# Kernel optimization log

Hardware: AMD Instinct MI355X
Metric: run time of the kernel (lower is better)

Reference implementation:

```python
import jax, jax.numpy as jnp
import numpy as np

B, N, C = 1, 131072, 128
BS, H = 32, 4          # block_size, num_heads
HD = C // H            # head_dim = 32
NB = N // BS           # num_blocks = 4096
NEG = -1e30            # stand-in for -inf (identical softmax result, safe grads)


def setup_inputs() -> dict:
    key = jax.random.key(0)
    ks = jax.random.split(key, 8)
    x = jax.random.normal(ks[0], (B, N, C), jnp.float32)
    edge_feats = jax.random.normal(ks[1], (NB, BS, BS + 1, 4), jnp.float32)
    # 0/1 connectivity mask; guarantee self (diagonal) and global-token column are attendable
    attn_mask = jax.random.randint(ks[2], (NB, BS, BS + 1), 0, 2).astype(jnp.int32)
    attn_mask = attn_mask.at[:, :, BS].set(1)
    d = jnp.arange(BS)
    attn_mask = attn_mask.at[:, d, d].set(1)
    # parameters (torch nn.Linear layout: weight [out, in])
    Wqkv = jax.random.normal(ks[3], (3 * C, C), jnp.float32) * (C ** -0.5)
    bqkv = jnp.zeros((3 * C,), jnp.float32)
    Wproj = jax.random.normal(ks[4], (C, C), jnp.float32) * (C ** -0.5)
    bproj = jnp.zeros((C,), jnp.float32)
    Wgate = jax.random.normal(ks[5], (H, 4), jnp.float32) * 0.01  # init std=0.01
    bgate = jnp.zeros((H,), jnp.float32)
    return dict(x=x, edge_feats=edge_feats, Wqkv=Wqkv, bqkv=bqkv,
                Wproj=Wproj, bproj=bproj, Wgate=Wgate, bgate=bgate,
                attn_mask=attn_mask)


def reference(x, edge_feats, Wqkv, bqkv, Wproj, bproj, Wgate, bgate, attn_mask):
    scale = HD ** -0.5
    x_blk = x.reshape(B, NB, BS, C)
    # global token per block = block mean
    block_node = x_blk.mean(axis=2, keepdims=True)          # [B,NB,1,C]
    kv = jnp.concatenate([x_blk, block_node], axis=2)       # [B,NB,BS+1,C]
    # qkv projections (slice the fused weight like the torch code slices outputs)
    q = (x_blk @ Wqkv[:C].T + bqkv[:C]).reshape(B, NB, BS, H, HD)
    k = (kv @ Wqkv[C:2 * C].T + bqkv[C:2 * C]).reshape(B, NB, BS + 1, H, HD)
    v = (kv @ Wqkv[2 * C:].T + bqkv[2 * C:]).reshape(B, NB, BS + 1, H, HD)
    scores = jnp.einsum('bnqhd,bnkhd->bnqkh', q, k) * scale  # [B,NB,BS,BS+1,H]
    # physics bias: overwrite global-token column and diagonal with (0,0,0,1)
    self_row = jnp.array([0.0, 0.0, 0.0, 1.0], jnp.float32)
    bp = jnp.broadcast_to(edge_feats[None], (B, NB, BS, BS + 1, 4))
    bp = bp.at[:, :, :, BS, :].set(self_row)
    d = jnp.arange(BS)
    bp = bp.at[:, :, d, d, :].set(self_row)
    scores = scores + bp[..., 3:4]                           # additive physics bias
    m = attn_mask[None, :, :, :, None] != 0                  # [1,NB,BS,BS+1,1]
    scores = jnp.where(m, scores, NEG)
    attn_probs = jax.nn.softmax(scores, axis=3)
    # additive edge gate (masked to 0 where disconnected)
    lew = jnp.where(m, bp @ Wgate.T + bgate, 0.0)            # [B,NB,BS,BS+1,H]
    combined = attn_probs + lew
    x_out = jnp.einsum('bnqkh,bnkhd->bnqhd', combined, v).reshape(B, N, C)
    return x_out @ Wproj.T + bproj
```

## Files before the change

kernel.cpp:

```cpp
#include <hip/hip_runtime.h>
#include <hip/hip_bf16.h>

#define NBLK 4096
#define BS 32
#define CH 128

typedef float f32x4 __attribute__((ext_vector_type(4)));
typedef short bf16x8 __attribute__((ext_vector_type(8)));
typedef unsigned short u16x4 __attribute__((ext_vector_type(4)));

__device__ __forceinline__ short f2b(float x) {
    union { float f; unsigned u; } c; c.f = x;
    unsigned r = c.u + 0x7fffu + ((c.u >> 16) & 1u);
    return (short)(r >> 16);
}
__device__ __forceinline__ float b2f(unsigned short h) {
    union { unsigned u; float f; } c; c.u = ((unsigned)h) << 16; return c.f;
}
__device__ __forceinline__ u16x4 pack4(f32x4 a) {
    u16x4 o;
    o[0] = (unsigned short)f2b(a[0]);
    o[1] = (unsigned short)f2b(a[1]);
    o[2] = (unsigned short)f2b(a[2]);
    o[3] = (unsigned short)f2b(a[3]);
    return o;
}

__global__ void convert_weights(const float* __restrict__ wqkv,
                                const float* __restrict__ wproj,
                                short* __restrict__ wsout) {
    int i = blockIdx.x * 256 + threadIdx.x;
    if (i < 3 * CH * CH) {
        wsout[i] = f2b(wqkv[i]);
    } else {
        int j = i - 3 * CH * CH;
        if (j < CH * CH) wsout[3 * CH * CH + j] = f2b(wproj[j]);
    }
}

__launch_bounds__(256, 4)
__global__ void fused_block_attn(
    const float* __restrict__ x,
    const float* __restrict__ edge_feats,
    const float* __restrict__ bqkv,
    const float* __restrict__ bproj,
    const float* __restrict__ wgate,
    const float* __restrict__ bgate,
    const int*   __restrict__ attn_mask,
    const short* __restrict__ wqkv_b,
    const short* __restrict__ wproj_b,
    float* __restrict__ out)
{
    const int b    = blockIdx.x;
    const int tid  = threadIdx.x;
    const int lane = tid & 63;
    const int w    = tid >> 6;
    const int lm   = lane & 15;
    const int g    = lane >> 4;
    const int ak   = g * 8;
    const int rb   = g * 4;

    __shared__ short regionA[32 * 136];
    __shared__ short qs[4 * 32 * 40];
    __shared__ short kc[4 * 32 * 40];
    __shared__ short vt[4 * 32 * 40];

    const float* xb = x + (size_t)b * BS * CH;
    #pragma unroll
    for (int it = 0; it < 4; ++it) {
        int idx = tid + it * 256;
        int r   = idx >> 5;
        int c4  = idx & 31;
        f32x4 t = ((const f32x4*)xb)[idx];
        *(u16x4*)&regionA[r * 136 + c4 * 4] = pack4(t);
    }
    __syncthreads();

    bf16x8 kvf[2][4];
    #pragma unroll
    for (int kk = 0; kk < 4; ++kk) {
        kvf[0][kk] = *(const bf16x8*)&regionA[lm * 136 + kk * 32 + ak];
        kvf[1][kk] = *(const bf16x8*)&regionA[(16 + lm) * 136 + kk * 32 + ak];
    }

    #pragma unroll
    for (int ntl = 0; ntl < 6; ++ntl) {
        const int nt = w * 6 + ntl;
        const int o0 = nt * 16;
        const short* wp = wqkv_b + (o0 + lm) * CH + ak;
        bf16x8 wf[4];
        #pragma unroll
        for (int kk = 0; kk < 4; ++kk) wf[kk] = *(const bf16x8*)(wp + kk * 32);

        const int h  = (o0 >> 5) & 3;
        if (nt < 16) {
            f32x4 a0 = *(const f32x4*)(bqkv + o0 + rb);
            f32x4 a1 = a0;
            #pragma unroll
            for (int kk = 0; kk < 4; ++kk) {
                a0 = __builtin_amdgcn_mfma_f32_16x16x32_bf16(wf[kk], kvf[0][kk], a0, 0, 0, 0);
                a1 = __builtin_amdgcn_mfma_f32_16x16x32_bf16(wf[kk], kvf[1][kk], a1, 0, 0, 0);
            }
            const int d0 = (o0 & 31) + rb;
            short* dst = ((nt < 8) ? qs : kc) + h * 1280;
            *(u16x4*)&dst[lm * 40 + d0]        = pack4(a0);
            *(u16x4*)&dst[(16 + lm) * 40 + d0] = pack4(a1);
        } else {
            float bv = bqkv[o0 + lm];
            f32x4 a0 = {bv, bv, bv, bv};
            f32x4 a1 = a0;
            #pragma unroll
            for (int kk = 0; kk < 4; ++kk) {
                a0 = __builtin_amdgcn_mfma_f32_16x16x32_bf16(kvf[0][kk], wf[kk], a0, 0, 0, 0);
                a1 = __builtin_amdgcn_mfma_f32_16x16x32_bf16(kvf[1][kk], wf[kk], a1, 0, 0, 0);
            }
            const int d0 = (o0 & 31) + lm;
            short* dst = vt + h * 1280;
            *(u16x4*)&dst[d0 * 40 + rb]      = pack4(a0);
            *(u16x4*)&dst[d0 * 40 + 16 + rb] = pack4(a1);
        }
    }
    __syncthreads();

    {
        const int h = w;
        const short* ksh = kc + h * 1280;
        const short* qsh = qs + h * 1280;
        bf16x8 af0 = *(const bf16x8*)&ksh[lm * 40 + ak];
        bf16x8 af1 = *(const bf16x8*)&ksh[(16 + lm) * 40 + ak];
        bf16x8 bf0 = *(const bf16x8*)&qsh[lm * 40 + ak];
        bf16x8 bf1 = *(const bf16x8*)&qsh[(16 + lm) * 40 + ak];
        f32x4 z = {0.f, 0.f, 0.f, 0.f};
        f32x4 s00 = __builtin_amdgcn_mfma_f32_16x16x32_bf16(af0, bf0, z, 0, 0, 0);
        f32x4 s10 = __builtin_amdgcn_mfma_f32_16x16x32_bf16(af1, bf0, z, 0, 0, 0);
        f32x4 s01 = __builtin_amdgcn_mfma_f32_16x16x32_bf16(af0, bf1, z, 0, 0, 0);
        f32x4 s11 = __builtin_amdgcn_mfma_f32_16x16x32_bf16(af1, bf1, z, 0, 0, 0);
        const float SC = 0.17677669529663689f;
        short* ch = kc + h * 1280;
        *(u16x4*)&ch[lm * 40 + rb]             = pack4(s00 * SC);
        *(u16x4*)&ch[lm * 40 + 16 + rb]        = pack4(s10 * SC);
        *(u16x4*)&ch[(16 + lm) * 40 + rb]      = pack4(s01 * SC);
        *(u16x4*)&ch[(16 + lm) * 40 + 16 + rb] = pack4(s11 * SC);
    }
    __syncthreads();

    {
        const int r    = tid >> 3;
        const int h    = (tid >> 1) & 3;
        const int half = tid & 1;
        short* ch = kc + h * 1280;

        bf16x8 t0 = *(const bf16x8*)&ch[r * 40 + half * 16];
        bf16x8 t1 = *(const bf16x8*)&ch[r * 40 + half * 16 + 8];
        float d[16];
        #pragma unroll
        for (int j = 0; j < 8; ++j) { d[j] = b2f((unsigned short)t0[j]); d[8 + j] = b2f((unsigned short)t1[j]); }

        float sd = 0.f;
        #pragma unroll
        for (int j = 0; j < 16; ++j) sd += d[j];
        sd += __shfl_xor(sd, 1);
        const float d32 = sd * 0.03125f;

        const float* efb = edge_feats + ((size_t)(b * BS + r)) * 33 * 4 + half * 64;
        const int*   mk  = attn_mask + (size_t)(b * BS + r) * 33 + half * 16;
        f32x4 wg = *(const f32x4*)(wgate + h * 4);
        float bg = bgate[h];

        float sc[16], lw[16];
        float mx = -3.0e38f;
        #pragma unroll
        for (int s = 0; s < 16; ++s) {
            int sg = half * 16 + s;
            f32x4 ef = *(const f32x4*)(efb + s * 4);
            if (sg == r) { ef[0] = 0.f; ef[1] = 0.f; ef[2] = 0.f; ef[3] = 1.f; }
            int m = mk[s];
            sc[s] = m ? (d[s] + ef[3]) : -1.0e30f;
            lw[s] = m ? (ef[0] * wg[0] + ef[1] * wg[1] + ef[2] * wg[2] + ef[3] * wg[3] + bg) : 0.f;
            mx = fmaxf(mx, sc[s]);
        }
        mx = fmaxf(mx, __shfl_xor(mx, 1));
        const float sc32 = d32 + 1.0f;
        mx = fmaxf(mx, sc32);

        float se = 0.f;
        #pragma unroll
        for (int s = 0; s < 16; ++s) {
            float e = __expf(sc[s] - mx);
            sc[s] = e;
            se += e;
        }
        const float e32 = __expf(sc32 - mx);
        const float tot = se + __shfl_xor(se, 1) + e32;
        const float rinv = 1.0f / tot;
        const float add32 = (e32 * rinv + (wg[3] + bg)) * 0.03125f;

        #pragma unroll
        for (int pk = 0; pk < 4; ++pk) {
            u16x4 o;
            #pragma unroll
            for (int j = 0; j < 4; ++j) {
                float v = sc[pk * 4 + j] * rinv + lw[pk * 4 + j] + add32;
                o[j] = (unsigned short)f2b(v);
            }
            *(u16x4*)&ch[r * 40 + half * 16 + pk * 4] = o;
        }
    }
    __syncthreads();

    {
        const int h = w;
        const short* ch  = kc + h * 1280;
        const short* vth = vt + h * 1280;
        bf16x8 av0 = *(const bf16x8*)&vth[lm * 40 + ak];
        bf16x8 av1 = *(const bf16x8*)&vth[(16 + lm) * 40 + ak];
        bf16x8 bc0 = *(const bf16x8*)&ch[lm * 40 + ak];
        bf16x8 bc1 = *(const bf16x8*)&ch[(16 + lm) * 40 + ak];
        f32x4 z = {0.f, 0.f, 0.f, 0.f};
        f32x4 x00 = __builtin_amdgcn_mfma_f32_16x16x32_bf16(av0, bc0, z, 0, 0, 0);
        f32x4 x10 = __builtin_amdgcn_mfma_f32_16x16x32_bf16(av1, bc0, z, 0, 0, 0);
        f32x4 x01 = __builtin_amdgcn_mfma_f32_16x16x32_bf16(av0, bc1, z, 0, 0, 0);
        f32x4 x11 = __builtin_amdgcn_mfma_f32_16x16x32_bf16(av1, bc1, z, 0, 0, 0);
        short* xob = regionA;
        *(u16x4*)&xob[lm * 136 + h * 32 + rb]             = pack4(x00);
        *(u16x4*)&xob[lm * 136 + h * 32 + 16 + rb]        = pack4(x10);
        *(u16x4*)&xob[(16 + lm) * 136 + h * 32 + rb]      = pack4(x01);
        *(u16x4*)&xob[(16 + lm) * 136 + h * 32 + 16 + rb] = pack4(x11);
    }
    __syncthreads();

    {
        const short* xob = regionA;
        bf16x8 a2[2][4];
        #pragma unroll
        for (int kk = 0; kk < 4; ++kk) {
            a2[0][kk] = *(const bf16x8*)&xob[lm * 136 + kk * 32 + ak];
            a2[1][kk] = *(const bf16x8*)&xob[(16 + lm) * 136 + kk * 32 + ak];
        }
        float* ob = out + (size_t)b * BS * CH;
        #pragma unroll
        for (int ntl = 0; ntl < 2; ++ntl) {
            int col = (w * 2 + ntl) * 16 + lm;
            float bias = bproj[col];
            f32x4 acc0 = {bias, bias, bias, bias};
            f32x4 acc1 = acc0;
            #pragma unroll
            for (int kk = 0; kk < 4; ++kk) {
                bf16x8 bfr = *(const bf16x8*)(wproj_b + col * CH + kk * 32 + ak);
                acc0 = __builtin_amdgcn_mfma_f32_16x16x32_bf16(a2[0][kk], bfr, acc0, 0, 0, 0);
                acc1 = __builtin_amdgcn_mfma_f32_16x16x32_bf16(a2[1][kk], bfr, acc1, 0, 0, 0);
            }
            #pragma unroll
            for (int j = 0; j < 4; ++j) {
                ob[(rb + j) * CH + col]      = acc0[j];
                ob[(16 + rb + j) * CH + col] = acc1[j];
            }
        }
    }
}

extern "C" void kernel_launch(void* const* d_in, const int* in_sizes, int n_in,
                              void* d_out, int out_size, void* d_ws, size_t ws_size,
                              hipStream_t stream) {
    const float* x          = (const float*)d_in[0];
    const float* edge_feats = (const float*)d_in[1];
    const float* Wqkv       = (const float*)d_in[2];
    const float* bqkv       = (const float*)d_in[3];
    const float* Wproj      = (const float*)d_in[4];
    const float* bproj      = (const float*)d_in[5];
    const float* Wgate      = (const float*)d_in[6];
    const float* bgate      = (const float*)d_in[7];
    const int*   attn_mask  = (const int*)d_in[8];
    float* out = (float*)d_out;
    short* wb  = (short*)d_ws;

    convert_weights<<<256, 256, 0, stream>>>(Wqkv, Wproj, wb);
    fused_block_attn<<<NBLK, 256, 0, stream>>>(
        x, edge_feats, bqkv, bproj, Wgate, bgate, attn_mask,
        wb, wb + 3 * CH * CH, out);
}
```

Baseline: 95.87 us.

## Give each wave one head end-to-end to drop most block barriers

Each wave now computes Q, K and V for its own head straight from global x, which is converted to bf16 in registers. Scores, softmax and PV then run wave-locally in XOR-swizzled shared-memory tiles, leaving only one __syncthreads before the output projection. The change also drops the softmax max-subtraction, prefetches the projection weights before the barrier, uses the builtin bf16 conversion, and raises launch bounds to 6 blocks per SM. The cost is redundant global reads of x by each wave, and exp overflow becomes possible if scores grow large.

```diff
diff --git a/kernel.cpp b/kernel.cpp
--- a/kernel.cpp
+++ b/kernel.cpp
@@ -10,20 +10,25 @@
 typedef unsigned short u16x4 __attribute__((ext_vector_type(4)));
 
 __device__ __forceinline__ short f2b(float x) {
-    union { float f; unsigned u; } c; c.f = x;
-    unsigned r = c.u + 0x7fffu + ((c.u >> 16) & 1u);
-    return (short)(r >> 16);
+    return __builtin_bit_cast(short, __float2bfloat16(x));
 }
 __device__ __forceinline__ float b2f(unsigned short h) {
     union { unsigned u; float f; } c; c.u = ((unsigned)h) << 16; return c.f;
 }
 __device__ __forceinline__ u16x4 pack4(f32x4 a) {
     u16x4 o;
-    o[0] = (unsigned short)f2b(a[0]);
-    o[1] = (unsigned short)f2b(a[1]);
-    o[2] = (unsigned short)f2b(a[2]);
-    o[3] = (unsigned short)f2b(a[3]);
+    o[0] = (unsigned short)f2b(a[0]); o[1] = (unsigned short)f2b(a[1]);
+    o[2] = (unsigned short)f2b(a[2]); o[3] = (unsigned short)f2b(a[3]);
     return o;
+}
+__device__ __forceinline__ bf16x8 pack8(f32x4 a, f32x4 b) {
+    bf16x8 o;
+    o[0] = f2b(a[0]); o[1] = f2b(a[1]); o[2] = f2b(a[2]); o[3] = f2b(a[3]);
+    o[4] = f2b(b[0]); o[5] = f2b(b[1]); o[6] = f2b(b[2]); o[7] = f2b(b[3]);
+    return o;
+}
+__device__ __forceinline__ int swz(int row, int col) {
+    return (row << 5) + ((((col >> 3) ^ ((row >> 1) & 3)) << 3) | (col & 7));
 }
 
 __global__ void convert_weights(const float* __restrict__ wqkv,
@@ -38,7 +43,7 @@
     }
 }
 
-__launch_bounds__(256, 4)
+__launch_bounds__(256, 6)
 __global__ void fused_block_attn(
     const float* __restrict__ x,
     const float* __restrict__ edge_feats,
@@ -60,195 +65,173 @@
     const int ak   = g * 8;
     const int rb   = g * 4;
 
-    __shared__ short regionA[32 * 136];
-    __shared__ short qs[4 * 32 * 40];
-    __shared__ short kc[4 * 32 * 40];
-    __shared__ short vt[4 * 32 * 40];
-
-    const float* xb = x + (size_t)b * BS * CH;
-    #pragma unroll
-    for (int it = 0; it < 4; ++it) {
-        int idx = tid + it * 256;
-        int r   = idx >> 5;
-        int c4  = idx & 31;
-        f32x4 t = ((const f32x4*)xb)[idx];
-        *(u16x4*)&regionA[r * 136 + c4 * 4] = pack4(t);
-    }
-    __syncthreads();
-
+    __shared__ short Rv[4096];
+    __shared__ short Rq[4096];
+    __shared__ short Rk[4096];
+    short* vt = Rv + w * 1024;
+    short* qc = Rq + w * 1024;
+    short* kc = Rk + w * 1024;
+
+    const float* xb = x + (size_t)b * (BS * CH);
     bf16x8 kvf[2][4];
     #pragma unroll
     for (int kk = 0; kk < 4; ++kk) {
-        kvf[0][kk] = *(const bf16x8*)&regionA[lm * 136 + kk * 32 + ak];
-        kvf[1][kk] = *(const bf16x8*)&regionA[(16 + lm) * 136 + kk * 32 + ak];
-    }
-
-    #pragma unroll
-    for (int ntl = 0; ntl < 6; ++ntl) {
-        const int nt = w * 6 + ntl;
-        const int o0 = nt * 16;
+        const float* p0 = xb + lm * CH + kk * 32 + ak;
+        const float* p1 = p0 + 16 * CH;
+        kvf[0][kk] = pack8(*(const f32x4*)p0, *(const f32x4*)(p0 + 4));
+        kvf[1][kk] = pack8(*(const f32x4*)p1, *(const f32x4*)(p1 + 4));
+    }
+
+    #pragma unroll
+    for (int t = 0; t < 4; ++t) {
+        const int o0 = ((t >> 1) ? CH : 0) + w * 32 + (t & 1) * 16;
         const short* wp = wqkv_b + (o0 + lm) * CH + ak;
         bf16x8 wf[4];
         #pragma unroll
         for (int kk = 0; kk < 4; ++kk) wf[kk] = *(const bf16x8*)(wp + kk * 32);
-
-        const int h  = (o0 >> 5) & 3;
-        if (nt < 16) {
-            f32x4 a0 = *(const f32x4*)(bqkv + o0 + rb);
-            f32x4 a1 = a0;
-            #pragma unroll
-            for (int kk = 0; kk < 4; ++kk) {
-                a0 = __builtin_amdgcn_mfma_f32_16x16x32_bf16(wf[kk], kvf[0][kk], a0, 0, 0, 0);
-                a1 = __builtin_amdgcn_mfma_f32_16x16x32_bf16(wf[kk], kvf[1][kk], a1, 0, 0, 0);
-            }
-            const int d0 = (o0 & 31) + rb;
-            short* dst = ((nt < 8) ? qs : kc) + h * 1280;
-            *(u16x4*)&dst[lm * 40 + d0]        = pack4(a0);
-            *(u16x4*)&dst[(16 + lm) * 40 + d0] = pack4(a1);
-        } else {
-            float bv = bqkv[o0 + lm];
-            f32x4 a0 = {bv, bv, bv, bv};
-            f32x4 a1 = a0;
-            #pragma unroll
-            for (int kk = 0; kk < 4; ++kk) {
-                a0 = __builtin_amdgcn_mfma_f32_16x16x32_bf16(kvf[0][kk], wf[kk], a0, 0, 0, 0);
-                a1 = __builtin_amdgcn_mfma_f32_16x16x32_bf16(kvf[1][kk], wf[kk], a1, 0, 0, 0);
-            }
-            const int d0 = (o0 & 31) + lm;
-            short* dst = vt + h * 1280;
-            *(u16x4*)&dst[d0 * 40 + rb]      = pack4(a0);
-            *(u16x4*)&dst[d0 * 40 + 16 + rb] = pack4(a1);
-        }
-    }
-    __syncthreads();
-
-    {
-        const int h = w;
-        const short* ksh = kc + h * 1280;
-        const short* qsh = qs + h * 1280;
-        bf16x8 af0 = *(const bf16x8*)&ksh[lm * 40 + ak];
-        bf16x8 af1 = *(const bf16x8*)&ksh[(16 + lm) * 40 + ak];
-        bf16x8 bf0 = *(const bf16x8*)&qsh[lm * 40 + ak];
-        bf16x8 bf1 = *(const bf16x8*)&qsh[(16 + lm) * 40 + ak];
+        f32x4 acc0 = *(const f32x4*)(bqkv + o0 + rb);
+        f32x4 acc1 = acc0;
+        #pragma unroll
+        for (int kk = 0; kk < 4; ++kk) {
+            acc0 = __builtin_amdgcn_mfma_f32_16x16x32_bf16(wf[kk], kvf[0][kk], acc0, 0, 0, 0);
+            acc1 = __builtin_amdgcn_mfma_f32_16x16x32_bf16(wf[kk], kvf[1][kk], acc1, 0, 0, 0);
+        }
+        short* dst = (t >> 1) ? kc : qc;
+        const int c0 = (t & 1) * 16 + rb;
+        *(u16x4*)&dst[swz(lm, c0)]      = pack4(acc0);
+        *(u16x4*)&dst[swz(16 + lm, c0)] = pack4(acc1);
+    }
+    #pragma unroll
+    for (int t = 0; t < 2; ++t) {
+        const int o0 = 2 * CH + w * 32 + t * 16;
+        const short* wp = wqkv_b + (o0 + lm) * CH + ak;
+        bf16x8 wf[4];
+        #pragma unroll
+        for (int kk = 0; kk < 4; ++kk) wf[kk] = *(const bf16x8*)(wp + kk * 32);
+        float bv = bqkv[o0 + lm];
+        f32x4 acc0 = {bv, bv, bv, bv};
+        f32x4 acc1 = acc0;
+        #pragma unroll
+        for (int kk = 0; kk < 4; ++kk) {
+            acc0 = __builtin_amdgcn_mfma_f32_16x16x32_bf16(kvf[0][kk], wf[kk], acc0, 0, 0, 0);
+            acc1 = __builtin_amdgcn_mfma_f32_16x16x32_bf16(kvf[1][kk], wf[kk], acc1, 0, 0, 0);
+        }
+        const int row = t * 16 + lm;
+        *(u16x4*)&vt[swz(row, rb)]      = pack4(acc0);
+        *(u16x4*)&vt[swz(row, 16 + rb)] = pack4(acc1);
+    }
+
+    {
+        bf16x8 af0 = *(const bf16x8*)&kc[swz(lm, ak)];
+        bf16x8 af1 = *(const bf16x8*)&kc[swz(16 + lm, ak)];
+        bf16x8 bq0 = *(const bf16x8*)&qc[swz(lm, ak)];
+        bf16x8 bq1 = *(const bf16x8*)&qc[swz(16 + lm, ak)];
         f32x4 z = {0.f, 0.f, 0.f, 0.f};
-        f32x4 s00 = __builtin_amdgcn_mfma_f32_16x16x32_bf16(af0, bf0, z, 0, 0, 0);
-        f32x4 s10 = __builtin_amdgcn_mfma_f32_16x16x32_bf16(af1, bf0, z, 0, 0, 0);
-        f32x4 s01 = __builtin_amdgcn_mfma_f32_16x16x32_bf16(af0, bf1, z, 0, 0, 0);
-        f32x4 s11 = __builtin_amdgcn_mfma_f32_16x16x32_bf16(af1, bf1, z, 0, 0, 0);
+        f32x4 s00 = __builtin_amdgcn_mfma_f32_16x16x32_bf16(af0, bq0, z, 0, 0, 0);
+        f32x4 s10 = __builtin_amdgcn_mfma_f32_16x16x32_bf16(af1, bq0, z, 0, 0, 0);
+        f32x4 s01 = __builtin_amdgcn_mfma_f32_16x16x32_bf16(af0, bq1, z, 0, 0, 0);
+        f32x4 s11 = __builtin_amdgcn_mfma_f32_16x16x32_bf16(af1, bq1, z, 0, 0, 0);
         const float SC = 0.17677669529663689f;
-        short* ch = kc + h * 1280;
-        *(u16x4*)&ch[lm * 40 + rb]             = pack4(s00 * SC);
-        *(u16x4*)&ch[lm * 40 + 16 + rb]        = pack4(s10 * SC);
-        *(u16x4*)&ch[(16 + lm) * 40 + rb]      = pack4(s01 * SC);
-        *(u16x4*)&ch[(16 + lm) * 40 + 16 + rb] = pack4(s11 * SC);
-    }
-    __syncthreads();
-
-    {
-        const int r    = tid >> 3;
-        const int h    = (tid >> 1) & 3;
-        const int half = tid & 1;
-        short* ch = kc + h * 1280;
-
-        bf16x8 t0 = *(const bf16x8*)&ch[r * 40 + half * 16];
-        bf16x8 t1 = *(const bf16x8*)&ch[r * 40 + half * 16 + 8];
-        float d[16];
-        #pragma unroll
-        for (int j = 0; j < 8; ++j) { d[j] = b2f((unsigned short)t0[j]); d[8 + j] = b2f((unsigned short)t1[j]); }
+        *(u16x4*)&kc[swz(lm, rb)]           = pack4(s00 * SC);
+        *(u16x4*)&kc[swz(lm, 16 + rb)]      = pack4(s10 * SC);
+        *(u16x4*)&kc[swz(16 + lm, rb)]      = pack4(s01 * SC);
+        *(u16x4*)&kc[swz(16 + lm, 16 + rb)] = pack4(s11 * SC);
+    }
+
+    {
+        const int r    = lane >> 1;
+        const int half = lane & 1;
+        bf16x8 t0 = *(const bf16x8*)&kc[swz(r, half * 16)];
+        bf16x8 t1 = *(const bf16x8*)&kc[swz(r, half * 16 + 8)];
 
         float sd = 0.f;
         #pragma unroll
-        for (int j = 0; j < 16; ++j) sd += d[j];
+        for (int j = 0; j < 8; ++j)
+            sd += b2f((unsigned short)t0[j]) + b2f((unsigned short)t1[j]);
         sd += __shfl_xor(sd, 1);
         const float d32 = sd * 0.03125f;
 
-        const float* efb = edge_feats + ((size_t)(b * BS + r)) * 33 * 4 + half * 64;
-        const int*   mk  = attn_mask + (size_t)(b * BS + r) * 33 + half * 16;
-        f32x4 wg = *(const f32x4*)(wgate + h * 4);
-        float bg = bgate[h];
-
-        float sc[16], lw[16];
-        float mx = -3.0e38f;
+        const float* efb = edge_feats + ((size_t)((b * BS + r) * 33 + half * 16)) * 4;
+        const int*   mkb = attn_mask + (size_t)(b * BS + r) * 33 + half * 16;
+        f32x4 wg = *(const f32x4*)(wgate + w * 4);
+        float bg = bgate[w];
+
+        float e[16], lw[16];
+        float se = 0.f;
         #pragma unroll
         for (int s = 0; s < 16; ++s) {
-            int sg = half * 16 + s;
+            float dv = (s < 8) ? b2f((unsigned short)t0[s]) : b2f((unsigned short)t1[s - 8]);
             f32x4 ef = *(const f32x4*)(efb + s * 4);
-            if (sg == r) { ef[0] = 0.f; ef[1] = 0.f; ef[2] = 0.f; ef[3] = 1.f; }
-            int m = mk[s];
-            sc[s] = m ? (d[s] + ef[3]) : -1.0e30f;
-            lw[s] = m ? (ef[0] * wg[0] + ef[1] * wg[1] + ef[2] * wg[2] + ef[3] * wg[3] + bg) : 0.f;
-            mx = fmaxf(mx, sc[s]);
-        }
-        mx = fmaxf(mx, __shfl_xor(mx, 1));
-        const float sc32 = d32 + 1.0f;
-        mx = fmaxf(mx, sc32);
-
-        float se = 0.f;
-        #pragma unroll
-        for (int s = 0; s < 16; ++s) {
-            float e = __expf(sc[s] - mx);
-            sc[s] = e;
-            se += e;
-        }
-        const float e32 = __expf(sc32 - mx);
+            bool diag = (half * 16 + s) == r;
+            float ef0 = diag ? 0.f : ef[0];
+            float ef1 = diag ? 0.f : ef[1];
+            float ef2 = diag ? 0.f : ef[2];
+            float ef3 = diag ? 1.f : ef[3];
+            int m = mkb[s];
+            lw[s] = m ? (ef0 * wg[0] + ef1 * wg[1] + ef2 * wg[2] + ef3 * wg[3] + bg) : 0.f;
+            e[s]  = m ? __expf(dv + ef3) : 0.f;
+            se += e[s];
+        }
+        const float e32 = __expf(d32 + 1.0f);
         const float tot = se + __shfl_xor(se, 1) + e32;
         const float rinv = 1.0f / tot;
-        const float add32 = (e32 * rinv + (wg[3] + bg)) * 0.03125f;
+        const float add32 = (e32 * rinv + wg[3] + bg) * 0.03125f;
 
         #pragma unroll
         for (int pk = 0; pk < 4; ++pk) {
-            u16x4 o;
+            f32x4 v;
             #pragma unroll
-            for (int j = 0; j < 4; ++j) {
-                float v = sc[pk * 4 + j] * rinv + lw[pk * 4 + j] + add32;
-                o[j] = (unsigned short)f2b(v);
-            }
-            *(u16x4*)&ch[r * 40 + half * 16 + pk * 4] = o;
-        }
-    }
-    __syncthreads();
-
-    {
-        const int h = w;
-        const short* ch  = kc + h * 1280;
-        const short* vth = vt + h * 1280;
-        bf16x8 av0 = *(const bf16x8*)&vth[lm * 40 + ak];
-        bf16x8 av1 = *(const bf16x8*)&vth[(16 + lm) * 40 + ak];
-        bf16x8 bc0 = *(const bf16x8*)&ch[lm * 40 + ak];
-        bf16x8 bc1 = *(const bf16x8*)&ch[(16 + lm) * 40 + ak];
+            for (int j = 0; j < 4; ++j)
+                v[j] = e[pk * 4 + j] * rinv + lw[pk * 4 + j] + add32;
+            *(u16x4*)&kc[swz(r, half * 16 + pk * 4)] = pack4(v);
+        }
+    }
+
+    {
+        bf16x8 av0 = *(const bf16x8*)&vt[swz(lm, ak)];
+        bf16x8 av1 = *(const bf16x8*)&vt[swz(16 + lm, ak)];
+        bf16x8 bc0 = *(const bf16x8*)&kc[swz(lm, ak)];
+        bf16x8 bc1 = *(const bf16x8*)&kc[swz(16 + lm, ak)];
         f32x4 z = {0.f, 0.f, 0.f, 0.f};
         f32x4 x00 = __builtin_amdgcn_mfma_f32_16x16x32_bf16(av0, bc0, z, 0, 0, 0);
         f32x4 x10 = __builtin_amdgcn_mfma_f32_16x16x32_bf16(av1, bc0, z, 0, 0, 0);
         f32x4 x01 = __builtin_amdgcn_mfma_f32_16x16x32_bf16(av0, bc1, z, 0, 0, 0);
         f32x4 x11 = __builtin_amdgcn_mfma_f32_16x16x32_bf16(av1, bc1, z, 0, 0, 0);
-        short* xob = regionA;
-        *(u16x4*)&xob[lm * 136 + h * 32 + rb]             = pack4(x00);
-        *(u16x4*)&xob[lm * 136 + h * 32 + 16 + rb]        = pack4(x10);
-        *(u16x4*)&xob[(16 + lm) * 136 + h * 32 + rb]      = pack4(x01);
-        *(u16x4*)&xob[(16 + lm) * 136 + h * 32 + 16 + rb] = pack4(x11);
+        *(u16x4*)&qc[swz(lm, rb)]           = pack4(x00);
+        *(u16x4*)&qc[swz(lm, 16 + rb)]      = pack4(x10);
+        *(u16x4*)&qc[swz(16 + lm, rb)]      = pack4(x01);
+        *(u16x4*)&qc[swz(16 + lm, 16 + rb)] = pack4(x11);
+    }
+
+    bf16x8 pw[2][4];
+    float pb[2];
+    #pragma unroll
+    for (int t = 0; t < 2; ++t) {
+        int col = w * 32 + t * 16 + lm;
+        pb[t] = bproj[col];
+        #pragma unroll
+        for (int kk = 0; kk < 4; ++kk)
+            pw[t][kk] = *(const bf16x8*)(wproj_b + col * CH + kk * 32 + ak);
     }
     __syncthreads();
 
     {
-        const short* xob = regionA;
         bf16x8 a2[2][4];
         #pragma unroll
         for (int kk = 0; kk < 4; ++kk) {
-            a2[0][kk] = *(const bf16x8*)&xob[lm * 136 + kk * 32 + ak];
-            a2[1][kk] = *(const bf16x8*)&xob[(16 + lm) * 136 + kk * 32 + ak];
+            a2[0][kk] = *(const bf16x8*)&Rq[kk * 1024 + swz(lm, ak)];
+            a2[1][kk] = *(const bf16x8*)&Rq[kk * 1024 + swz(16 + lm, ak)];
         }
         float* ob = out + (size_t)b * BS * CH;
         #pragma unroll
-        for (int ntl = 0; ntl < 2; ++ntl) {
-            int col = (w * 2 + ntl) * 16 + lm;
-            float bias = bproj[col];
-            f32x4 acc0 = {bias, bias, bias, bias};
+        for (int t = 0; t < 2; ++t) {
+            int col = w * 32 + t * 16 + lm;
+            f32x4 acc0 = {pb[t], pb[t], pb[t], pb[t]};
             f32x4 acc1 = acc0;
             #pragma unroll
             for (int kk = 0; kk < 4; ++kk) {
-                bf16x8 bfr = *(const bf16x8*)(wproj_b + col * CH + kk * 32 + ak);
-                acc0 = __builtin_amdgcn_mfma_f32_16x16x32_bf16(a2[0][kk], bfr, acc0, 0, 0, 0);
-                acc1 = __builtin_amdgcn_mfma_f32_16x16x32_bf16(a2[1][kk], bfr, acc1, 0, 0, 0);
+                acc0 = __builtin_amdgcn_mfma_f32_16x16x32_bf16(a2[0][kk], pw[t][kk], acc0, 0, 0, 0);
+                acc1 = __builtin_amdgcn_mfma_f32_16x16x32_bf16(a2[1][kk], pw[t][kk], acc1, 0, 0, 0);
             }
             #pragma unroll
             for (int j = 0; j < 4; ++j) {
```

New measurement: 138.8 us. 44.8% more time.
